# Kernel tuning notes

Measured on AMD Instinct MI355X. Metric: run time of the kernel, lower is better.

The kernel has to match this reference:

```python
import jax, jax.numpy as jnp
import numpy as np

N_NODES = 50000
N_EDGES = 1600000
IN_CH = 128
OUT_CH = 128
MAX_NORM = 1.0


def setup_inputs() -> dict:
    key = jax.random.key(0)
    k1, k2, k3, k4 = jax.random.split(key, 4)
    x = jax.random.normal(k1, (N_NODES, IN_CH), dtype=jnp.float32)
    edge_index = jax.random.randint(k2, (2, N_EDGES), 0, N_NODES, dtype=jnp.int64)
    # GCNConv lin: weight [out, in] (kaiming-ish init), bias [out] zeros-ish
    W = jax.random.normal(k3, (OUT_CH, IN_CH), dtype=jnp.float32) * (1.0 / np.sqrt(IN_CH))
    b = jax.random.normal(k4, (OUT_CH,), dtype=jnp.float32) * 0.01
    return {"x": x, "edge_index": edge_index, "W": W, "b": b}


def _renorm_cols(W, max_norm):
    # torch.renorm(W, p=2, dim=1, maxnorm): each slice along dim 1 (column of [out,in])
    # is rescaled so its L2 norm <= max_norm.
    norms = jnp.sqrt(jnp.sum(W * W, axis=0, keepdims=True))  # [1, in]
    scale = jnp.where(norms > max_norm, max_norm / norms, 1.0)
    return W * scale


def reference(x, edge_index, W, b):
    N = x.shape[0]
    Wn = _renorm_cols(W, MAX_NORM)
    # Linear transform first (as PyG GCNConv does): h = x @ W^T
    h = jnp.einsum('ni,oi->no', x, Wn)  # [N, out]

    # Add self loops
    row = jnp.concatenate([edge_index[0], jnp.arange(N, dtype=edge_index.dtype)])
    col = jnp.concatenate([edge_index[1], jnp.arange(N, dtype=edge_index.dtype)])

    # Symmetric normalization: deg over destination (col), edge weights = 1
    ones = jnp.ones(row.shape[0], dtype=h.dtype)
    deg = jax.ops.segment_sum(ones, col, num_segments=N)
    deg_inv_sqrt = jnp.where(deg > 0, jax.lax.rsqrt(deg), 0.0)
    norm = deg_inv_sqrt[row] * deg_inv_sqrt[col]  # [E+N]

    # Gather source features, scale, scatter-add to destinations
    msgs = h[row] * norm[:, None]  # [E+N, out]
    out = jax.ops.segment_sum(msgs, col, num_segments=N)
    return out + b
```

## Files before the change

### kernel.cpp

```cpp
#include <hip/hip_runtime.h>

#define N_NODES 50000
#define N_EDGES 1600000
#define CH 128
#define NB 196
#define CHUNK_E 2048
#define NCHUNK 784

#define WS_WBF     0
#define WS_CNT     32768
#define WS_OFFS    647424
#define WS_BTOT    1262080
#define WS_BSTART  1262864
#define WS_ROWPTR  1263656
#define WS_DINV    1463664
#define WS_SCL     1663664
#define WS_SRC     1863664
#define WS_EQ      8263664
#define WS_ESTASH  14663664

typedef __bf16 bf16x8 __attribute__((ext_vector_type(8)));
typedef float f32x4 __attribute__((ext_vector_type(4)));

__device__ __forceinline__ unsigned int pack_bf16(float a, float b) {
    unsigned int ua = __builtin_bit_cast(unsigned int, a);
    unsigned int ub = __builtin_bit_cast(unsigned int, b);
    ua = (ua + 0x7FFFu + ((ua >> 16) & 1u)) >> 16;
    ub = (ub + 0x7FFFu + ((ub >> 16) & 1u)) >> 16;
    return ua | (ub << 16);
}

__global__ void k_prep(const float* __restrict__ W, unsigned int* __restrict__ Wbf) {
    __shared__ float s_scale[128];
    int t = threadIdx.x;
    float s = 0.f;
    for (int o = 0; o < CH; ++o) { float w = W[o * CH + t]; s += w * w; }
    s_scale[t] = (s > 1.0f) ? rsqrtf(s) : 1.0f;
    __syncthreads();
    for (int k16 = 0; k16 < 64; ++k16) {
        float a = W[t * CH + 2 * k16]     * s_scale[2 * k16];
        float b = W[t * CH + 2 * k16 + 1] * s_scale[2 * k16 + 1];
        Wbf[t * 64 + k16] = pack_bf16(a, b);
    }
}

__global__ __launch_bounds__(256) void k_part1(const int* __restrict__ eidx,
                                               unsigned int* __restrict__ estash,
                                               int* __restrict__ cnt) {
    __shared__ int lc[256];
    __shared__ int s_st;
    int t = threadIdx.x, c = blockIdx.x;
    lc[t] = 0;
    if (t < 64) {
        int v = eidx[2 * t + 1];
        unsigned long long m = __ballot(v == 0);
        if (t == 0) s_st = (m == ~0ull) ? 2 : 1;
    }
    __syncthreads();
    int st = s_st;
    long base = (long)c * CHUNK_E;
    #pragma unroll
    for (int i = 0; i < CHUNK_E / 256; ++i) {
        long e = base + i * 256 + t;
        if (e < N_EDGES) {
            int row = eidx[(size_t)st * (size_t)e];
            int col = eidx[(size_t)st * (size_t)(N_EDGES + e)];
            estash[e] = (unsigned int)row | ((unsigned int)col << 16);
            atomicAdd(&lc[col >> 8], 1);
        }
    }
    __syncthreads();
    if (t < NB) cnt[t * NCHUNK + c] = lc[t];
}

__global__ __launch_bounds__(256) void k_coff1(const int* __restrict__ cnt,
                                               int* __restrict__ offs,
                                               int* __restrict__ btot) {
    __shared__ int sh[256];
    int t = threadIdx.x, b = blockIdx.x;
    const int4* cp = (const int4*)(cnt + b * NCHUNK);
    int4 v = make_int4(0, 0, 0, 0);
    if (t < NCHUNK / 4) v = cp[t];
    int s = v.x + v.y + v.z + v.w;
    sh[t] = s;
    __syncthreads();
    for (int off = 1; off < 256; off <<= 1) {
        int u = (t >= off) ? sh[t - off] : 0;
        __syncthreads();
        sh[t] += u;
        __syncthreads();
    }
    int base = sh[t] - s;
    if (t < NCHUNK / 4) {
        int4 o;
        o.x = base;
        o.y = o.x + v.x;
        o.z = o.y + v.y;
        o.w = o.z + v.z;
        ((int4*)(offs + b * NCHUNK))[t] = o;
    }
    if (t == 255) btot[b] = sh[255];
}

__global__ __launch_bounds__(256) void k_coff2(const int* __restrict__ btot,
                                               int* __restrict__ bstart) {
    __shared__ int sh[256];
    int t = threadIdx.x;
    int v = (t < NB) ? btot[t] : 0;
    sh[t] = v;
    __syncthreads();
    for (int off = 1; off < 256; off <<= 1) {
        int u = (t >= off) ? sh[t - off] : 0;
        __syncthreads();
        sh[t] += u;
        __syncthreads();
    }
    int excl = sh[t] - v;
    if (t < NB) bstart[t] = excl;
    if (t == NB - 1) bstart[NB] = excl + v;
}

__global__ __launch_bounds__(256) void k_part2(const unsigned int* __restrict__ estash,
                                               const int* __restrict__ offs,
                                               const int* __restrict__ bstart,
                                               unsigned int* __restrict__ ebuf) {
    __shared__ int lcur[256];
    int t = threadIdx.x, c = blockIdx.x;
    if (t < NB) lcur[t] = bstart[t] + offs[t * NCHUNK + c];
    __syncthreads();
    long base = (long)c * CHUNK_E;
    #pragma unroll
    for (int i = 0; i < CHUNK_E / 256; ++i) {
        long e = base + i * 256 + t;
        if (e < N_EDGES) {
            unsigned int u = estash[e];
            int bb = u >> 24;
            int pos = atomicAdd(&lcur[bb], 1);
            ebuf[pos] = (u & 0xFFFFu) | (((u >> 16) & 0xFFu) << 16);
        }
    }
}

__global__ __launch_bounds__(256) void k_sort(const unsigned int* __restrict__ ebuf,
                                              const int* __restrict__ bstart,
                                              int* __restrict__ rowptr,
                                              float* __restrict__ dinv,
                                              int* __restrict__ src) {
    __shared__ int ldeg[256];
    __shared__ int lcur[256];
    __shared__ int sh[256];
    int t = threadIdx.x, b = blockIdx.x;
    int i0 = bstart[b], i1 = bstart[b + 1];
    ldeg[t] = 0;
    __syncthreads();
    for (int i = i0 + t; i < i1; i += 256) {
        unsigned int p = ebuf[i];
        atomicAdd(&ldeg[(p >> 16) & 255], 1);
    }
    __syncthreads();
    int d = ldeg[t];
    sh[t] = d;
    __syncthreads();
    for (int off = 1; off < 256; off <<= 1) {
        int u = (t >= off) ? sh[t - off] : 0;
        __syncthreads();
        sh[t] += u;
        __syncthreads();
    }
    int local_rp = i0 + sh[t] - d;
    int n = (b << 8) + t;
    if (n < N_NODES) {
        rowptr[n] = local_rp;
        dinv[n] = rsqrtf((float)(d + 1));
    }
    if (b == NB - 1 && t == 0) rowptr[N_NODES] = N_EDGES;
    lcur[t] = local_rp;
    __syncthreads();
    for (int i = i0 + t; i < i1; i += 256) {
        unsigned int p = ebuf[i];
        int pos = atomicAdd(&lcur[(p >> 16) & 255], 1);
        src[pos] = (int)(p & 0xFFFFu);
    }
}

__global__ __launch_bounds__(256) void k_gemm(const float* __restrict__ x,
                                              const unsigned int* __restrict__ Wbf,
                                              const float* __restrict__ dinv,
                                              unsigned int* __restrict__ q8,
                                              float* __restrict__ scl) {
    __shared__ uint4 SMEM[3072];
    uint4* xs = SMEM;
    uint4* wsl = SMEM + 1024;
    float* scratch = (float*)SMEM;
    int t = threadIdx.x;
    int base = blockIdx.x * 64;
    #pragma unroll
    for (int it = 0; it < 4; ++it) {
        int idx = it * 256 + t;
        int r = idx >> 4, c16 = idx & 15;
        int n = base + r;
        float4 v0 = make_float4(0.f, 0.f, 0.f, 0.f), v1 = v0;
        if (n < N_NODES) {
            v0 = *(const float4*)&x[(size_t)n * CH + c16 * 8];
            v1 = *(const float4*)&x[(size_t)n * CH + c16 * 8 + 4];
        }
        uint4 p;
        p.x = pack_bf16(v0.x, v0.y); p.y = pack_bf16(v0.z, v0.w);
        p.z = pack_bf16(v1.x, v1.y); p.w = pack_bf16(v1.z, v1.w);
        xs[r * 16 + (c16 ^ (r & 7))] = p;
    }
    const uint4* wb4 = (const uint4*)Wbf;
    #pragma unroll
    for (int it = 0; it < 8; ++it) {
        int idx = it * 256 + t;
        int o = idx >> 4, c16 = idx & 15;
        wsl[o * 16 + (c16 ^ (o & 7))] = wb4[idx];
    }
    __syncthreads();
    int w = t >> 6, l = t & 63;
    int lrow = w * 16 + (l & 15);
    int hi = l >> 4;
    bf16x8 a[4];
    #pragma unroll
    for (int ks = 0; ks < 4; ++ks) {
        int c16 = ks * 4 + hi;
        a[ks] = __builtin_bit_cast(bf16x8, xs[lrow * 16 + (c16 ^ (lrow & 7))]);
    }
    float di[4];
    #pragma unroll
    for (int r = 0; r < 4; ++r) {
        int n = base + w * 16 + hi * 4 + r;
        di[r] = (n < N_NODES) ? dinv[n] : 0.f;
    }
    float vals[8][4];
    #pragma unroll
    for (int tc = 0; tc < 8; ++tc) {
        int col = tc * 16 + (l & 15);
        f32x4 acc = {0.f, 0.f, 0.f, 0.f};
        #pragma unroll
        for (int ks = 0; ks < 4; ++ks) {
            int c16 = ks * 4 + hi;
            bf16x8 bf = __builtin_bit_cast(bf16x8, wsl[col * 16 + (c16 ^ (col & 7))]);
            acc = __builtin_amdgcn_mfma_f32_16x16x32_bf16(a[ks], bf, acc, 0, 0, 0);
        }
        #pragma unroll
        for (int r = 0; r < 4; ++r) vals[tc][r] = acc[r] * di[r];
    }
    __syncthreads();
    #pragma unroll
    for (int tc = 0; tc < 8; ++tc) {
        int col = tc * 16 + (l & 15);
        #pragma unroll
        for (int r = 0; r < 4; ++r) {
            int rl = w * 16 + hi * 4 + r;
            scratch[rl * 132 + col] = vals[tc][r];
        }
    }
    __syncthreads();
    int rl = t >> 2, q = t & 3;
    const float4* rp = (const float4*)&scratch[rl * 132 + q * 32];
    float4 f[8];
    float m = 0.f;
    #pragma unroll
    for (int k = 0; k < 8; ++k) {
        f[k] = rp[k];
        m = fmaxf(m, fmaxf(fmaxf(fabsf(f[k].x), fabsf(f[k].y)),
                           fmaxf(fabsf(f[k].z), fabsf(f[k].w))));
    }
    m = fmaxf(m, __shfl_xor(m, 1));
    m = fmaxf(m, __shfl_xor(m, 2));
    float sc = m * (1.0f / 127.0f);
    float inv = (m > 0.f) ? (127.0f / m) : 0.f;
    int n = base + rl;
    if (n < N_NODES) {
        unsigned int u[8];
        #pragma unroll
        for (int k = 0; k < 8; ++k) {
            int b0 = __float2int_rn(f[k].x * inv);
            int b1 = __float2int_rn(f[k].y * inv);
            int b2 = __float2int_rn(f[k].z * inv);
            int b3 = __float2int_rn(f[k].w * inv);
            u[k] = (unsigned int)(b0 & 255) | ((unsigned int)(b1 & 255) << 8) |
                   ((unsigned int)(b2 & 255) << 16) | ((unsigned int)(b3 & 255) << 24);
        }
        uint4* qp = (uint4*)&q8[(size_t)n * 32 + q * 8];
        qp[0] = make_uint4(u[0], u[1], u[2], u[3]);
        qp[1] = make_uint4(u[4], u[5], u[6], u[7]);
        if (q == 0) scl[n] = sc;
    }
}

__global__ __launch_bounds__(256) void k_gather(const int* __restrict__ rowptr,
                                                const int* __restrict__ src,
                                                const unsigned int* __restrict__ q8,
                                                const float* __restrict__ scl,
                                                const float* __restrict__ dinv,
                                                const float* __restrict__ b,
                                                float* __restrict__ out) {
    int t = threadIdx.x;
    int wid = t >> 6, lane = t & 63;
    int half = lane >> 5, lc = lane & 31;
    int n = blockIdx.x * 4 + wid;
    if (n >= N_NODES) return;
    int j0 = rowptr[n], j1 = rowptr[n + 1];
    float a0 = 0.f, a1 = 0.f, a2 = 0.f, a3 = 0.f;
    int jj = j0;
    for (; jj + 8 <= j1; jj += 8) {
        #pragma unroll
        for (int k = 0; k < 4; ++k) {
            int r = src[jj + 2 * k + half];
            float sc = scl[r];
            unsigned int v = q8[(size_t)r * 32 + lc];
            a0 = fmaf((float)(signed char)(v), sc, a0);
            a1 = fmaf((float)(signed char)(v >> 8), sc, a1);
            a2 = fmaf((float)(signed char)(v >> 16), sc, a2);
            a3 = fmaf((float)(signed char)(v >> 24), sc, a3);
        }
    }
    for (; jj + 2 <= j1; jj += 2) {
        int r = src[jj + half];
        float sc = scl[r];
        unsigned int v = q8[(size_t)r * 32 + lc];
        a0 = fmaf((float)(signed char)(v), sc, a0);
        a1 = fmaf((float)(signed char)(v >> 8), sc, a1);
        a2 = fmaf((float)(signed char)(v >> 16), sc, a2);
        a3 = fmaf((float)(signed char)(v >> 24), sc, a3);
    }
    if (jj < j1 && half == 0) {
        int r = src[jj];
        float sc = scl[r];
        unsigned int v = q8[(size_t)r * 32 + lc];
        a0 = fmaf((float)(signed char)(v), sc, a0);
        a1 = fmaf((float)(signed char)(v >> 8), sc, a1);
        a2 = fmaf((float)(signed char)(v >> 16), sc, a2);
        a3 = fmaf((float)(signed char)(v >> 24), sc, a3);
    }
    a0 += __shfl_xor(a0, 32);
    a1 += __shfl_xor(a1, 32);
    a2 += __shfl_xor(a2, 32);
    a3 += __shfl_xor(a3, 32);
    if (half == 0) {
        float di = dinv[n];
        float sc = scl[n];
        unsigned int v = q8[(size_t)n * 32 + lc];
        float4 bv = *(const float4*)&b[4 * lc];
        float4 o;
        o.x = (a0 + (float)(signed char)(v) * sc) * di + bv.x;
        o.y = (a1 + (float)(signed char)(v >> 8) * sc) * di + bv.y;
        o.z = (a2 + (float)(signed char)(v >> 16) * sc) * di + bv.z;
        o.w = (a3 + (float)(signed char)(v >> 24) * sc) * di + bv.w;
        *(float4*)&out[(size_t)n * CH + 4 * lc] = o;
    }
}

extern "C" void kernel_launch(void* const* d_in, const int* in_sizes, int n_in,
                              void* d_out, int out_size, void* d_ws, size_t ws_size,
                              hipStream_t stream) {
    const float* x = (const float*)d_in[0];
    const int* eidx = (const int*)d_in[1];
    const float* W = (const float*)d_in[2];
    const float* b = (const float*)d_in[3];
    float* out = (float*)d_out;

    char* ws = (char*)d_ws;
    unsigned int* Wbf    = (unsigned int*)(ws + WS_WBF);
    int*   cnt           = (int*)(ws + WS_CNT);
    int*   offs          = (int*)(ws + WS_OFFS);
    int*   btot          = (int*)(ws + WS_BTOT);
    int*   bstart        = (int*)(ws + WS_BSTART);
    int*   rowptr        = (int*)(ws + WS_ROWPTR);
    float* dinv          = (float*)(ws + WS_DINV);
    float* sclp          = (float*)(ws + WS_SCL);
    int*   srcarr        = (int*)(ws + WS_SRC);
    unsigned int* ebuf   = (unsigned int*)(ws + WS_EQ);
    unsigned int* q8     = (unsigned int*)(ws + WS_EQ);
    unsigned int* estash = (unsigned int*)(ws + WS_ESTASH);

    k_prep<<<1, 128, 0, stream>>>(W, Wbf);
    k_part1<<<NCHUNK, 256, 0, stream>>>(eidx, estash, cnt);
    k_coff1<<<NB, 256, 0, stream>>>(cnt, offs, btot);
    k_coff2<<<1, 256, 0, stream>>>(btot, bstart);
    k_part2<<<NCHUNK, 256, 0, stream>>>(estash, offs, bstart, ebuf);
    k_sort<<<NB, 256, 0, stream>>>(ebuf, bstart, rowptr, dinv, srcarr);
    k_gemm<<<(N_NODES + 63) / 64, 256, 0, stream>>>(x, Wbf, dinv, q8, sclp);
    k_gather<<<(N_NODES + 3) / 4, 256, 0, stream>>>(rowptr, srcarr, q8, sclp, dinv, b, out);
}
```

Baseline: 119.1 us.

## Fuse CSR-build kernels into one cooperative kernel; deepen gather load batching

Merges six preprocessing kernels (weight renorm, partition count, two scans, scatter, per-bucket sort) into one cooperative launch of 196 blocks that uses grid-wide barriers between phases, removing five kernel launch gaps. Each block now handles four edge chunks serially, so there is less parallelism within the partition phases. The gather kernel also issues eight index and feature loads before doing the FMAs, to keep more memory requests in flight, and uses 32-bit index math.

```diff
diff --git a/kernel.cpp b/kernel.cpp
--- a/kernel.cpp
+++ b/kernel.cpp
@@ -1,4 +1,7 @@
 #include <hip/hip_runtime.h>
+#include <hip/hip_cooperative_groups.h>
+
+namespace cg = cooperative_groups;
 
 #define N_NODES 50000
 #define N_EDGES 1600000
@@ -30,27 +33,18 @@
     return ua | (ub << 16);
 }
 
-__global__ void k_prep(const float* __restrict__ W, unsigned int* __restrict__ Wbf) {
+__global__ __launch_bounds__(256) void k_pipeline(
+        const float* __restrict__ W, const int* __restrict__ eidx,
+        unsigned int* __restrict__ Wbf, unsigned int* __restrict__ estash,
+        int* __restrict__ cnt, int* __restrict__ offs, int* __restrict__ btot,
+        int* __restrict__ bstart, unsigned int* __restrict__ ebuf,
+        int* __restrict__ rowptr, float* __restrict__ dinv, int* __restrict__ src) {
+    cg::grid_group grid = cg::this_grid();
+    __shared__ int shA[256], shB[256], shC[256];
+    __shared__ int s_st;
     __shared__ float s_scale[128];
-    int t = threadIdx.x;
-    float s = 0.f;
-    for (int o = 0; o < CH; ++o) { float w = W[o * CH + t]; s += w * w; }
-    s_scale[t] = (s > 1.0f) ? rsqrtf(s) : 1.0f;
-    __syncthreads();
-    for (int k16 = 0; k16 < 64; ++k16) {
-        float a = W[t * CH + 2 * k16]     * s_scale[2 * k16];
-        float b = W[t * CH + 2 * k16 + 1] * s_scale[2 * k16 + 1];
-        Wbf[t * 64 + k16] = pack_bf16(a, b);
-    }
-}
-
-__global__ __launch_bounds__(256) void k_part1(const int* __restrict__ eidx,
-                                               unsigned int* __restrict__ estash,
-                                               int* __restrict__ cnt) {
-    __shared__ int lc[256];
-    __shared__ int s_st;
-    int t = threadIdx.x, c = blockIdx.x;
-    lc[t] = 0;
+    int t = threadIdx.x, bid = blockIdx.x;
+
     if (t < 64) {
         int v = eidx[2 * t + 1];
         unsigned long long m = __ballot(v == 0);
@@ -58,128 +52,139 @@
     }
     __syncthreads();
     int st = s_st;
-    long base = (long)c * CHUNK_E;
-    #pragma unroll
-    for (int i = 0; i < CHUNK_E / 256; ++i) {
-        long e = base + i * 256 + t;
-        if (e < N_EDGES) {
-            int row = eidx[(size_t)st * (size_t)e];
-            int col = eidx[(size_t)st * (size_t)(N_EDGES + e)];
-            estash[e] = (unsigned int)row | ((unsigned int)col << 16);
-            atomicAdd(&lc[col >> 8], 1);
-        }
-    }
-    __syncthreads();
-    if (t < NB) cnt[t * NCHUNK + c] = lc[t];
-}
-
-__global__ __launch_bounds__(256) void k_coff1(const int* __restrict__ cnt,
-                                               int* __restrict__ offs,
-                                               int* __restrict__ btot) {
-    __shared__ int sh[256];
-    int t = threadIdx.x, b = blockIdx.x;
-    const int4* cp = (const int4*)(cnt + b * NCHUNK);
-    int4 v = make_int4(0, 0, 0, 0);
-    if (t < NCHUNK / 4) v = cp[t];
-    int s = v.x + v.y + v.z + v.w;
-    sh[t] = s;
-    __syncthreads();
-    for (int off = 1; off < 256; off <<= 1) {
-        int u = (t >= off) ? sh[t - off] : 0;
-        __syncthreads();
-        sh[t] += u;
-        __syncthreads();
-    }
-    int base = sh[t] - s;
-    if (t < NCHUNK / 4) {
-        int4 o;
-        o.x = base;
-        o.y = o.x + v.x;
-        o.z = o.y + v.y;
-        o.w = o.z + v.z;
-        ((int4*)(offs + b * NCHUNK))[t] = o;
-    }
-    if (t == 255) btot[b] = sh[255];
-}
-
-__global__ __launch_bounds__(256) void k_coff2(const int* __restrict__ btot,
-                                               int* __restrict__ bstart) {
-    __shared__ int sh[256];
-    int t = threadIdx.x;
-    int v = (t < NB) ? btot[t] : 0;
-    sh[t] = v;
-    __syncthreads();
-    for (int off = 1; off < 256; off <<= 1) {
-        int u = (t >= off) ? sh[t - off] : 0;
-        __syncthreads();
-        sh[t] += u;
-        __syncthreads();
-    }
-    int excl = sh[t] - v;
-    if (t < NB) bstart[t] = excl;
-    if (t == NB - 1) bstart[NB] = excl + v;
-}
-
-__global__ __launch_bounds__(256) void k_part2(const unsigned int* __restrict__ estash,
-                                               const int* __restrict__ offs,
-                                               const int* __restrict__ bstart,
-                                               unsigned int* __restrict__ ebuf) {
-    __shared__ int lcur[256];
-    int t = threadIdx.x, c = blockIdx.x;
-    if (t < NB) lcur[t] = bstart[t] + offs[t * NCHUNK + c];
-    __syncthreads();
-    long base = (long)c * CHUNK_E;
-    #pragma unroll
-    for (int i = 0; i < CHUNK_E / 256; ++i) {
-        long e = base + i * 256 + t;
-        if (e < N_EDGES) {
-            unsigned int u = estash[e];
-            int bb = u >> 24;
-            int pos = atomicAdd(&lcur[bb], 1);
-            ebuf[pos] = (u & 0xFFFFu) | (((u >> 16) & 0xFFu) << 16);
-        }
-    }
-}
-
-__global__ __launch_bounds__(256) void k_sort(const unsigned int* __restrict__ ebuf,
-                                              const int* __restrict__ bstart,
-                                              int* __restrict__ rowptr,
-                                              float* __restrict__ dinv,
-                                              int* __restrict__ src) {
-    __shared__ int ldeg[256];
-    __shared__ int lcur[256];
-    __shared__ int sh[256];
-    int t = threadIdx.x, b = blockIdx.x;
-    int i0 = bstart[b], i1 = bstart[b + 1];
-    ldeg[t] = 0;
-    __syncthreads();
-    for (int i = i0 + t; i < i1; i += 256) {
-        unsigned int p = ebuf[i];
-        atomicAdd(&ldeg[(p >> 16) & 255], 1);
-    }
-    __syncthreads();
-    int d = ldeg[t];
-    sh[t] = d;
-    __syncthreads();
-    for (int off = 1; off < 256; off <<= 1) {
-        int u = (t >= off) ? sh[t - off] : 0;
-        __syncthreads();
-        sh[t] += u;
-        __syncthreads();
-    }
-    int local_rp = i0 + sh[t] - d;
-    int n = (b << 8) + t;
-    if (n < N_NODES) {
-        rowptr[n] = local_rp;
-        dinv[n] = rsqrtf((float)(d + 1));
-    }
-    if (b == NB - 1 && t == 0) rowptr[N_NODES] = N_EDGES;
-    lcur[t] = local_rp;
-    __syncthreads();
-    for (int i = i0 + t; i < i1; i += 256) {
-        unsigned int p = ebuf[i];
-        int pos = atomicAdd(&lcur[(p >> 16) & 255], 1);
-        src[pos] = (int)(p & 0xFFFFu);
+
+    if (bid == 0) {
+        if (t < 128) {
+            float s = 0.f;
+            for (int o = 0; o < CH; ++o) { float w = W[o * CH + t]; s += w * w; }
+            s_scale[t] = (s > 1.0f) ? rsqrtf(s) : 1.0f;
+        }
+        __syncthreads();
+        if (t < 128) {
+            for (int k16 = 0; k16 < 64; ++k16) {
+                float a = W[t * CH + 2 * k16]     * s_scale[2 * k16];
+                float b = W[t * CH + 2 * k16 + 1] * s_scale[2 * k16 + 1];
+                Wbf[t * 64 + k16] = pack_bf16(a, b);
+            }
+        }
+        __syncthreads();
+    }
+    for (int p = 0; p < 4; ++p) {
+        int c = bid + p * NB;
+        shA[t] = 0;
+        __syncthreads();
+        long base = (long)c * CHUNK_E;
+        #pragma unroll
+        for (int i = 0; i < CHUNK_E / 256; ++i) {
+            long e = base + i * 256 + t;
+            if (e < N_EDGES) {
+                int row = eidx[(size_t)st * (size_t)e];
+                int col = eidx[(size_t)st * (size_t)(N_EDGES + e)];
+                estash[e] = (unsigned int)row | ((unsigned int)col << 16);
+                atomicAdd(&shA[col >> 8], 1);
+            }
+        }
+        __syncthreads();
+        if (t < NB) cnt[t * NCHUNK + c] = shA[t];
+        __syncthreads();
+    }
+    grid.sync();
+
+    {
+        int b = bid;
+        const int4* cp = (const int4*)(cnt + b * NCHUNK);
+        int4 v = make_int4(0, 0, 0, 0);
+        if (t < NCHUNK / 4) v = cp[t];
+        int s = v.x + v.y + v.z + v.w;
+        shC[t] = s;
+        __syncthreads();
+        for (int off = 1; off < 256; off <<= 1) {
+            int u = (t >= off) ? shC[t - off] : 0;
+            __syncthreads();
+            shC[t] += u;
+            __syncthreads();
+        }
+        int base = shC[t] - s;
+        if (t < NCHUNK / 4) {
+            int4 o;
+            o.x = base;
+            o.y = o.x + v.x;
+            o.z = o.y + v.y;
+            o.w = o.z + v.z;
+            ((int4*)(offs + b * NCHUNK))[t] = o;
+        }
+        if (t == 255) btot[b] = shC[255];
+    }
+    grid.sync();
+
+    if (bid == 0) {
+        int v = (t < NB) ? btot[t] : 0;
+        shC[t] = v;
+        __syncthreads();
+        for (int off = 1; off < 256; off <<= 1) {
+            int u = (t >= off) ? shC[t - off] : 0;
+            __syncthreads();
+            shC[t] += u;
+            __syncthreads();
+        }
+        int excl = shC[t] - v;
+        if (t < NB) bstart[t] = excl;
+        if (t == NB - 1) bstart[NB] = excl + v;
+    }
+    grid.sync();
+
+    for (int p = 0; p < 4; ++p) {
+        int c = bid + p * NB;
+        if (t < NB) shB[t] = bstart[t] + offs[t * NCHUNK + c];
+        __syncthreads();
+        long base = (long)c * CHUNK_E;
+        #pragma unroll
+        for (int i = 0; i < CHUNK_E / 256; ++i) {
+            long e = base + i * 256 + t;
+            if (e < N_EDGES) {
+                unsigned int u = estash[e];
+                int bb = u >> 24;
+                int pos = atomicAdd(&shB[bb], 1);
+                ebuf[pos] = (u & 0xFFFFu) | (((u >> 16) & 0xFFu) << 16);
+            }
+        }
+        __syncthreads();
+    }
+    grid.sync();
+
+    {
+        int b = bid;
+        int i0 = bstart[b], i1 = bstart[b + 1];
+        shA[t] = 0;
+        __syncthreads();
+        for (int i = i0 + t; i < i1; i += 256) {
+            unsigned int p = ebuf[i];
+            atomicAdd(&shA[(p >> 16) & 255], 1);
+        }
+        __syncthreads();
+        int d = shA[t];
+        shC[t] = d;
+        __syncthreads();
+        for (int off = 1; off < 256; off <<= 1) {
+            int u = (t >= off) ? shC[t - off] : 0;
+            __syncthreads();
+            shC[t] += u;
+            __syncthreads();
+        }
+        int local_rp = i0 + shC[t] - d;
+        int n = (b << 8) + t;
+        if (n < N_NODES) {
+            rowptr[n] = local_rp;
+            dinv[n] = rsqrtf((float)(d + 1));
+        }
+        if (b == NB - 1 && t == 0) rowptr[N_NODES] = N_EDGES;
+        shB[t] = local_rp;
+        __syncthreads();
+        for (int i = i0 + t; i < i1; i += 256) {
+            unsigned int p = ebuf[i];
+            int pos = atomicAdd(&shB[(p >> 16) & 255], 1);
+            src[pos] = (int)(p & 0xFFFFu);
+        }
     }
 }
 
@@ -305,22 +310,29 @@
     int j0 = rowptr[n], j1 = rowptr[n + 1];
     float a0 = 0.f, a1 = 0.f, a2 = 0.f, a3 = 0.f;
     int jj = j0;
-    for (; jj + 8 <= j1; jj += 8) {
-        #pragma unroll
-        for (int k = 0; k < 4; ++k) {
-            int r = src[jj + 2 * k + half];
-            float sc = scl[r];
-            unsigned int v = q8[(size_t)r * 32 + lc];
-            a0 = fmaf((float)(signed char)(v), sc, a0);
-            a1 = fmaf((float)(signed char)(v >> 8), sc, a1);
-            a2 = fmaf((float)(signed char)(v >> 16), sc, a2);
-            a3 = fmaf((float)(signed char)(v >> 24), sc, a3);
+    for (; jj + 16 <= j1; jj += 16) {
+        int rs[8];
+        #pragma unroll
+        for (int k = 0; k < 8; ++k) rs[k] = src[jj + 2 * k + half];
+        float ss[8];
+        unsigned int vs[8];
+        #pragma unroll
+        for (int k = 0; k < 8; ++k) {
+            ss[k] = scl[rs[k]];
+            vs[k] = q8[((unsigned)rs[k] << 5) + lc];
+        }
+        #pragma unroll
+        for (int k = 0; k < 8; ++k) {
+            a0 = fmaf((float)(signed char)(vs[k]), ss[k], a0);
+            a1 = fmaf((float)(signed char)(vs[k] >> 8), ss[k], a1);
+            a2 = fmaf((float)(signed char)(vs[k] >> 16), ss[k], a2);
+            a3 = fmaf((float)(signed char)(vs[k] >> 24), ss[k], a3);
         }
     }
     for (; jj + 2 <= j1; jj += 2) {
         int r = src[jj + half];
         float sc = scl[r];
-        unsigned int v = q8[(size_t)r * 32 + lc];
+        unsigned int v = q8[((unsigned)r << 5) + lc];
         a0 = fmaf((float)(signed char)(v), sc, a0);
         a1 = fmaf((float)(signed char)(v >> 8), sc, a1);
         a2 = fmaf((float)(signed char)(v >> 16), sc, a2);
@@ -329,7 +341,7 @@
     if (jj < j1 && half == 0) {
         int r = src[jj];
         float sc = scl[r];
-        unsigned int v = q8[(size_t)r * 32 + lc];
+        unsigned int v = q8[((unsigned)r << 5) + lc];
         a0 = fmaf((float)(signed char)(v), sc, a0);
         a1 = fmaf((float)(signed char)(v >> 8), sc, a1);
         a2 = fmaf((float)(signed char)(v >> 16), sc, a2);
@@ -342,7 +354,7 @@
     if (half == 0) {
         float di = dinv[n];
         float sc = scl[n];
-        unsigned int v = q8[(size_t)n * 32 + lc];
+        unsigned int v = q8[((unsigned)n << 5) + lc];
         float4 bv = *(const float4*)&b[4 * lc];
         float4 o;
         o.x = (a0 + (float)(signed char)(v) * sc) * di + bv.x;
@@ -376,12 +388,11 @@
     unsigned int* q8     = (unsigned int*)(ws + WS_EQ);
     unsigned int* estash = (unsigned int*)(ws + WS_ESTASH);
 
-    k_prep<<<1, 128, 0, stream>>>(W, Wbf);
-    k_part1<<<NCHUNK, 256, 0, stream>>>(eidx, estash, cnt);
-    k_coff1<<<NB, 256, 0, stream>>>(cnt, offs, btot);
-    k_coff2<<<1, 256, 0, stream>>>(btot, bstart);
-    k_part2<<<NCHUNK, 256, 0, stream>>>(estash, offs, bstart, ebuf);
-    k_sort<<<NB, 256, 0, stream>>>(ebuf, bstart, rowptr, dinv, srcarr);
+    void* args[] = {(void*)&W, (void*)&eidx, (void*)&Wbf, (void*)&estash,
+                    (void*)&cnt, (void*)&offs, (void*)&btot, (void*)&bstart,
+                    (void*)&ebuf, (void*)&rowptr, (void*)&dinv, (void*)&srcarr};
+    hipLaunchCooperativeKernel((const void*)k_pipeline, dim3(NB), dim3(256),
+                               args, 0, stream);
     k_gemm<<<(N_NODES + 63) / 64, 256, 0, stream>>>(x, Wbf, dinv, q8, sclp);
     k_gather<<<(N_NODES + 3) / 4, 256, 0, stream>>>(rowptr, srcarr, q8, sclp, dinv, b, out);
 }
```

New measurement: 230.6 us. 1.94x slower.

## Split gather into two channel halves and fold bucket-offset scan into consumers

Applied to the files above, without the earlier changes.

The int8 feature table is split into two 64-channel halves stored in separate arrays, and the gather runs twice, once per half. Each half's table (3.2 MB) is meant to fit better in cache, and each wavefront now handles four edges at a time with 16 lanes per row. The separate single-block bucket-offset scan kernel is removed and its prefix sum is recomputed redundantly inside k_part2 and k_sort, saving a launch. The cost is reading src, scl and rowptr twice, and extra scan work in every block of k_part2.

```diff
diff --git a/kernel.cpp b/kernel.cpp
--- a/kernel.cpp
+++ b/kernel.cpp
@@ -11,13 +11,15 @@
 #define WS_CNT     32768
 #define WS_OFFS    647424
 #define WS_BTOT    1262080
-#define WS_BSTART  1262864
 #define WS_ROWPTR  1263656
 #define WS_DINV    1463664
 #define WS_SCL     1663664
 #define WS_SRC     1863664
 #define WS_EQ      8263664
 #define WS_ESTASH  14663664
+
+#define Q8LO_OFF   WS_EQ
+#define Q8HI_OFF   (WS_EQ + 3200000)
 
 typedef __bf16 bf16x8 __attribute__((ext_vector_type(8)));
 typedef float f32x4 __attribute__((ext_vector_type(4)));
@@ -102,31 +104,22 @@
     if (t == 255) btot[b] = sh[255];
 }
 
-__global__ __launch_bounds__(256) void k_coff2(const int* __restrict__ btot,
-                                               int* __restrict__ bstart) {
-    __shared__ int sh[256];
-    int t = threadIdx.x;
-    int v = (t < NB) ? btot[t] : 0;
-    sh[t] = v;
-    __syncthreads();
-    for (int off = 1; off < 256; off <<= 1) {
-        int u = (t >= off) ? sh[t - off] : 0;
-        __syncthreads();
-        sh[t] += u;
-        __syncthreads();
-    }
-    int excl = sh[t] - v;
-    if (t < NB) bstart[t] = excl;
-    if (t == NB - 1) bstart[NB] = excl + v;
-}
-
 __global__ __launch_bounds__(256) void k_part2(const unsigned int* __restrict__ estash,
                                                const int* __restrict__ offs,
-                                               const int* __restrict__ bstart,
+                                               const int* __restrict__ btot,
                                                unsigned int* __restrict__ ebuf) {
-    __shared__ int lcur[256];
+    __shared__ int shB[256], shC[256];
     int t = threadIdx.x, c = blockIdx.x;
-    if (t < NB) lcur[t] = bstart[t] + offs[t * NCHUNK + c];
+    int v = (t < NB) ? btot[t] : 0;
+    shC[t] = v;
+    __syncthreads();
+    for (int off = 1; off < 256; off <<= 1) {
+        int u = (t >= off) ? shC[t - off] : 0;
+        __syncthreads();
+        shC[t] += u;
+        __syncthreads();
+    }
+    if (t < NB) shB[t] = (shC[t] - v) + offs[t * NCHUNK + c];
     __syncthreads();
     long base = (long)c * CHUNK_E;
     #pragma unroll
@@ -135,50 +128,60 @@
         if (e < N_EDGES) {
             unsigned int u = estash[e];
             int bb = u >> 24;
-            int pos = atomicAdd(&lcur[bb], 1);
+            int pos = atomicAdd(&shB[bb], 1);
             ebuf[pos] = (u & 0xFFFFu) | (((u >> 16) & 0xFFu) << 16);
         }
     }
 }
 
 __global__ __launch_bounds__(256) void k_sort(const unsigned int* __restrict__ ebuf,
-                                              const int* __restrict__ bstart,
+                                              const int* __restrict__ btot,
                                               int* __restrict__ rowptr,
                                               float* __restrict__ dinv,
                                               int* __restrict__ src) {
-    __shared__ int ldeg[256];
-    __shared__ int lcur[256];
-    __shared__ int sh[256];
+    __shared__ int shA[256], shB[256], shC[256];
+    __shared__ int s_i0, s_i1;
     int t = threadIdx.x, b = blockIdx.x;
-    int i0 = bstart[b], i1 = bstart[b + 1];
-    ldeg[t] = 0;
+    int v = (t < NB) ? btot[t] : 0;
+    shC[t] = v;
+    __syncthreads();
+    for (int off = 1; off < 256; off <<= 1) {
+        int u = (t >= off) ? shC[t - off] : 0;
+        __syncthreads();
+        shC[t] += u;
+        __syncthreads();
+    }
+    if (t == b) { s_i0 = shC[t] - v; s_i1 = shC[t]; }
+    __syncthreads();
+    int i0 = s_i0, i1 = s_i1;
+    shA[t] = 0;
     __syncthreads();
     for (int i = i0 + t; i < i1; i += 256) {
         unsigned int p = ebuf[i];
-        atomicAdd(&ldeg[(p >> 16) & 255], 1);
-    }
-    __syncthreads();
-    int d = ldeg[t];
-    sh[t] = d;
+        atomicAdd(&shA[(p >> 16) & 255], 1);
+    }
+    __syncthreads();
+    int d = shA[t];
+    shC[t] = d;
     __syncthreads();
     for (int off = 1; off < 256; off <<= 1) {
-        int u = (t >= off) ? sh[t - off] : 0;
-        __syncthreads();
-        sh[t] += u;
-        __syncthreads();
-    }
-    int local_rp = i0 + sh[t] - d;
+        int u = (t >= off) ? shC[t - off] : 0;
+        __syncthreads();
+        shC[t] += u;
+        __syncthreads();
+    }
+    int local_rp = i0 + shC[t] - d;
     int n = (b << 8) + t;
     if (n < N_NODES) {
         rowptr[n] = local_rp;
         dinv[n] = rsqrtf((float)(d + 1));
     }
     if (b == NB - 1 && t == 0) rowptr[N_NODES] = N_EDGES;
-    lcur[t] = local_rp;
+    shB[t] = local_rp;
     __syncthreads();
     for (int i = i0 + t; i < i1; i += 256) {
         unsigned int p = ebuf[i];
-        int pos = atomicAdd(&lcur[(p >> 16) & 255], 1);
+        int pos = atomicAdd(&shB[(p >> 16) & 255], 1);
         src[pos] = (int)(p & 0xFFFFu);
     }
 }
@@ -186,7 +189,8 @@
 __global__ __launch_bounds__(256) void k_gemm(const float* __restrict__ x,
                                               const unsigned int* __restrict__ Wbf,
                                               const float* __restrict__ dinv,
-                                              unsigned int* __restrict__ q8,
+                                              unsigned int* __restrict__ q8lo,
+                                              unsigned int* __restrict__ q8hi,
                                               float* __restrict__ scl) {
     __shared__ uint4 SMEM[3072];
     uint4* xs = SMEM;
@@ -283,73 +287,73 @@
             u[k] = (unsigned int)(b0 & 255) | ((unsigned int)(b1 & 255) << 8) |
                    ((unsigned int)(b2 & 255) << 16) | ((unsigned int)(b3 & 255) << 24);
         }
-        uint4* qp = (uint4*)&q8[(size_t)n * 32 + q * 8];
-        qp[0] = make_uint4(u[0], u[1], u[2], u[3]);
-        qp[1] = make_uint4(u[4], u[5], u[6], u[7]);
+        unsigned int* qp = (q < 2 ? q8lo : q8hi) + ((size_t)n << 4) + (q & 1) * 8;
+        ((uint4*)qp)[0] = make_uint4(u[0], u[1], u[2], u[3]);
+        ((uint4*)qp)[1] = make_uint4(u[4], u[5], u[6], u[7]);
         if (q == 0) scl[n] = sc;
     }
 }
 
 __global__ __launch_bounds__(256) void k_gather(const int* __restrict__ rowptr,
                                                 const int* __restrict__ src,
-                                                const unsigned int* __restrict__ q8,
+                                                const unsigned int* __restrict__ q8p,
                                                 const float* __restrict__ scl,
                                                 const float* __restrict__ dinv,
-                                                const float* __restrict__ b,
-                                                float* __restrict__ out) {
+                                                const float* __restrict__ bias,
+                                                float* __restrict__ out, int choff) {
     int t = threadIdx.x;
     int wid = t >> 6, lane = t & 63;
-    int half = lane >> 5, lc = lane & 31;
+    int quar = lane >> 4, lq = lane & 15;
     int n = blockIdx.x * 4 + wid;
     if (n >= N_NODES) return;
     int j0 = rowptr[n], j1 = rowptr[n + 1];
     float a0 = 0.f, a1 = 0.f, a2 = 0.f, a3 = 0.f;
     int jj = j0;
-    for (; jj + 8 <= j1; jj += 8) {
-        #pragma unroll
-        for (int k = 0; k < 4; ++k) {
-            int r = src[jj + 2 * k + half];
-            float sc = scl[r];
-            unsigned int v = q8[(size_t)r * 32 + lc];
-            a0 = fmaf((float)(signed char)(v), sc, a0);
-            a1 = fmaf((float)(signed char)(v >> 8), sc, a1);
-            a2 = fmaf((float)(signed char)(v >> 16), sc, a2);
-            a3 = fmaf((float)(signed char)(v >> 24), sc, a3);
-        }
-    }
-    for (; jj + 2 <= j1; jj += 2) {
-        int r = src[jj + half];
-        float sc = scl[r];
-        unsigned int v = q8[(size_t)r * 32 + lc];
+    for (; jj + 16 <= j1; jj += 16) {
+        int rs[4];
+        #pragma unroll
+        for (int g = 0; g < 4; ++g) rs[g] = src[jj + g * 4 + quar];
+        float ss[4];
+        unsigned int vs[4];
+        #pragma unroll
+        for (int g = 0; g < 4; ++g) {
+            ss[g] = scl[rs[g]];
+            vs[g] = q8p[((unsigned)rs[g] << 4) + lq];
+        }
+        #pragma unroll
+        for (int g = 0; g < 4; ++g) {
+            a0 = fmaf((float)(signed char)(vs[g]), ss[g], a0);
+            a1 = fmaf((float)(signed char)(vs[g] >> 8), ss[g], a1);
+            a2 = fmaf((float)(signed char)(vs[g] >> 16), ss[g], a2);
+            a3 = fmaf((float)(signed char)(vs[g] >> 24), ss[g], a3);
+        }
+    }
+    for (; jj < j1; jj += 4) {
+        int idx = jj + quar;
+        bool ok = idx < j1;
+        int r = ok ? src[idx] : 0;
+        float sc = ok ? scl[r] : 0.f;
+        unsigned int v = q8p[((unsigned)r << 4) + lq];
         a0 = fmaf((float)(signed char)(v), sc, a0);
         a1 = fmaf((float)(signed char)(v >> 8), sc, a1);
         a2 = fmaf((float)(signed char)(v >> 16), sc, a2);
         a3 = fmaf((float)(signed char)(v >> 24), sc, a3);
     }
-    if (jj < j1 && half == 0) {
-        int r = src[jj];
-        float sc = scl[r];
-        unsigned int v = q8[(size_t)r * 32 + lc];
-        a0 = fmaf((float)(signed char)(v), sc, a0);
-        a1 = fmaf((float)(signed char)(v >> 8), sc, a1);
-        a2 = fmaf((float)(signed char)(v >> 16), sc, a2);
-        a3 = fmaf((float)(signed char)(v >> 24), sc, a3);
-    }
-    a0 += __shfl_xor(a0, 32);
-    a1 += __shfl_xor(a1, 32);
-    a2 += __shfl_xor(a2, 32);
-    a3 += __shfl_xor(a3, 32);
-    if (half == 0) {
+    a0 += __shfl_xor(a0, 16); a0 += __shfl_xor(a0, 32);
+    a1 += __shfl_xor(a1, 16); a1 += __shfl_xor(a1, 32);
+    a2 += __shfl_xor(a2, 16); a2 += __shfl_xor(a2, 32);
+    a3 += __shfl_xor(a3, 16); a3 += __shfl_xor(a3, 32);
+    if (quar == 0) {
         float di = dinv[n];
         float sc = scl[n];
-        unsigned int v = q8[(size_t)n * 32 + lc];
-        float4 bv = *(const float4*)&b[4 * lc];
+        unsigned int v = q8p[((unsigned)n << 4) + lq];
+        float4 bv = *(const float4*)&bias[choff + 4 * lq];
         float4 o;
         o.x = (a0 + (float)(signed char)(v) * sc) * di + bv.x;
         o.y = (a1 + (float)(signed char)(v >> 8) * sc) * di + bv.y;
         o.z = (a2 + (float)(signed char)(v >> 16) * sc) * di + bv.z;
         o.w = (a3 + (float)(signed char)(v >> 24) * sc) * di + bv.w;
-        *(float4*)&out[(size_t)n * CH + 4 * lc] = o;
+        *(float4*)&out[(size_t)n * CH + choff + 4 * lq] = o;
     }
 }
 
@@ -367,21 +371,21 @@
     int*   cnt           = (int*)(ws + WS_CNT);
     int*   offs          = (int*)(ws + WS_OFFS);
     int*   btot          = (int*)(ws + WS_BTOT);
-    int*   bstart        = (int*)(ws + WS_BSTART);
     int*   rowptr        = (int*)(ws + WS_ROWPTR);
     float* dinv          = (float*)(ws + WS_DINV);
     float* sclp          = (float*)(ws + WS_SCL);
     int*   srcarr        = (int*)(ws + WS_SRC);
     unsigned int* ebuf   = (unsigned int*)(ws + WS_EQ);
-    unsigned int* q8     = (unsigned int*)(ws + WS_EQ);
+    unsigned int* q8lo   = (unsigned int*)(ws + Q8LO_OFF);
+    unsigned int* q8hi   = (unsigned int*)(ws + Q8HI_OFF);
     unsigned int* estash = (unsigned int*)(ws + WS_ESTASH);
 
     k_prep<<<1, 128, 0, stream>>>(W, Wbf);
     k_part1<<<NCHUNK, 256, 0, stream>>>(eidx, estash, cnt);
     k_coff1<<<NB, 256, 0, stream>>>(cnt, offs, btot);
-    k_coff2<<<1, 256, 0, stream>>>(btot, bstart);
-    k_part2<<<NCHUNK, 256, 0, stream>>>(estash, offs, bstart, ebuf);
-    k_sort<<<NB, 256, 0, stream>>>(ebuf, bstart, rowptr, dinv, srcarr);
-    k_gemm<<<(N_NODES + 63) / 64, 256, 0, stream>>>(x, Wbf, dinv, q8, sclp);
-    k_gather<<<(N_NODES + 3) / 4, 256, 0, stream>>>(rowptr, srcarr, q8, sclp, dinv, b, out);
-}
+    k_part2<<<NCHUNK, 256, 0, stream>>>(estash, offs, btot, ebuf);
+    k_sort<<<NB, 256, 0, stream>>>(ebuf, btot, rowptr, dinv, srcarr);
+    k_gemm<<<(N_NODES + 63) / 64, 256, 0, stream>>>(x, Wbf, dinv, q8lo, q8hi, sclp);
+    k_gather<<<(N_NODES + 3) / 4, 256, 0, stream>>>(rowptr, srcarr, q8lo, sclp, dinv, b, out, 0);
+    k_gather<<<(N_NODES + 3) / 4, 256, 0, stream>>>(rowptr, srcarr, q8hi, sclp, dinv, b, out, 64);
+}
```

After: 141.1 us. +18.4%, slower.
